# Kernel optimization log

Measured on AMD Instinct MI355X. Metric: run time of the kernel, lower is better.

Reference implementation:

```python
import jax, jax.numpy as jnp
import numpy as np
import math

D = 1024
H = 16
HD = D // H


def setup_inputs() -> dict:
    key = jax.random.key(0)
    ks = jax.random.split(key, 12)
    B, L = 2, 2048
    s = 1.0 / math.sqrt(D)
    inp = {
        "q": jax.random.normal(ks[0], (B, L, D), jnp.float32),
        "k": jax.random.normal(ks[1], (B, L, D), jnp.float32),
        "v": jax.random.normal(ks[2], (B, L, D), jnp.float32),
        "Wq": jax.random.normal(ks[3], (D, D), jnp.float32) * s,
        "bq": jnp.zeros((D,), jnp.float32),
        "Wk": jax.random.normal(ks[4], (D, D), jnp.float32) * s,
        "bk": jnp.zeros((D,), jnp.float32),
        "Wv": jax.random.normal(ks[5], (D, D), jnp.float32) * s,
        "bv": jnp.zeros((D,), jnp.float32),
        "Wo": jax.random.normal(ks[6], (D, D), jnp.float32) * s,
        "bo": jnp.zeros((D,), jnp.float32),
        "P": jax.random.normal(ks[7], (H, H), jnp.float32),  # logit_proj_pre
    }
    return inp


def _split_heads(x, B, L):
    # [B,L,D] -> [B,H,L,HD]
    return x.reshape(B, L, H, HD).transpose(0, 2, 1, 3)


def reference(q, k, v, Wq, bq, Wk, bk, Wv, bv, Wo, bo, P):
    B, L, _ = q.shape
    qh = _split_heads(q @ Wq.T + bq, B, L)
    kh = _split_heads(k @ Wk.T + bk, B, L)
    vh = _split_heads(v @ Wv.T + bv, B, L)
    # raw per-head logits [B,H,L,L]
    logits = jnp.einsum("bhld,bhmd->bhlm", qh, kh) / math.sqrt(HD)
    # talking-heads mixing across heads (pre-softmax)
    logits = jnp.einsum("bhlm,hg->bglm", logits, P)
    attn = jax.nn.softmax(logits, axis=-1)
    out = jnp.einsum("bhlm,bhmd->bhld", attn, vh)  # [B,H,L,HD]
    out = out.transpose(0, 2, 1, 3).reshape(B, L, D)
    return out @ Wo.T + bo
```

## Files before the change

### kernel.cpp

```cpp
#include <hip/hip_runtime.h>

#define D_  1024
#define H_  16
#define HD_ 64
#define L_  2048
#define B_  2
#define M_  (B_*L_)

typedef float f32x4  __attribute__((ext_vector_type(4)));
typedef short bf16x4 __attribute__((ext_vector_type(4)));
typedef short bf16x8 __attribute__((ext_vector_type(8)));

#define SRAW_PITCH 18
#define VS_PITCH   36

__device__ __forceinline__ float bf2f(short s) {
    return __uint_as_float(((unsigned int)(unsigned short)s) << 16);
}
__device__ __forceinline__ short f2bf(float f) {
    unsigned u = __float_as_uint(f);
    unsigned r = (u + 0x7FFFu + ((u >> 16) & 1u)) >> 16;
    return (short)r;
}
__device__ __forceinline__ void block_sync() {
    asm volatile("s_waitcnt lgkmcnt(0)" ::: "memory");
    __builtin_amdgcn_sched_barrier(0);
    __builtin_amdgcn_s_barrier();
    __builtin_amdgcn_sched_barrier(0);
}

__global__ __launch_bounds__(256) void proj_mfma(
    const float* __restrict__ q, const float* __restrict__ k, const float* __restrict__ v,
    const float* __restrict__ Wq, const float* __restrict__ bq,
    const float* __restrict__ Wk, const float* __restrict__ bk,
    const float* __restrict__ Wv, const float* __restrict__ bv,
    short* __restrict__ qh, short* __restrict__ qlo,
    short* __restrict__ kh, short* __restrict__ vht)
{
    const int z = blockIdx.z;
    const float* X    = (z == 0) ? q  : (z == 1) ? k  : v;
    const float* W    = (z == 0) ? Wq : (z == 1) ? Wk : Wv;
    const float* bias = (z == 0) ? bq : (z == 1) ? bk : bv;

    __shared__ short Ws[128][40];
    __shared__ short Xs[128][40];

    const int tid  = threadIdx.x;
    const int w    = tid >> 6, lane = tid & 63;
    const int l16  = lane & 15, qq = lane >> 4;
    const int m0   = blockIdx.x * 128;
    const int n0   = blockIdx.y * 128;
    const int ar0  = 64 * (w & 1);
    const int br0  = 64 * (w >> 1);

    f32x4 acc[4][4] = {};

    for (int k0 = 0; k0 < D_; k0 += 32) {
        #pragma unroll
        for (int i = 0; i < 4; ++i) {
            int fidx = i * 256 + tid;
            int r = fidx >> 3, c = fidx & 7;
            float4 wv4 = *(const float4*)(W + (size_t)(n0 + r) * D_ + k0 + c * 4);
            float4 xv4 = *(const float4*)(X + (size_t)(m0 + r) * D_ + k0 + c * 4);
            bf16x4 wb = { f2bf(wv4.x), f2bf(wv4.y), f2bf(wv4.z), f2bf(wv4.w) };
            bf16x4 xb = { f2bf(xv4.x), f2bf(xv4.y), f2bf(xv4.z), f2bf(xv4.w) };
            *(bf16x4*)&Ws[r][c * 4] = wb;
            *(bf16x4*)&Xs[r][c * 4] = xb;
        }
        __syncthreads();
        bf16x8 af[4], bfv[4];
        #pragma unroll
        for (int i = 0; i < 4; ++i) {
            const short* Ab = (z < 2) ? &Ws[ar0 + 16 * i + l16][qq * 8]
                                      : &Xs[ar0 + 16 * i + l16][qq * 8];
            const short* Bb = (z < 2) ? &Xs[br0 + 16 * i + l16][qq * 8]
                                      : &Ws[br0 + 16 * i + l16][qq * 8];
            af[i]  = *(const bf16x8*)Ab;
            bfv[i] = *(const bf16x8*)Bb;
        }
        #pragma unroll
        for (int i = 0; i < 4; ++i)
            #pragma unroll
            for (int j = 0; j < 4; ++j)
                acc[i][j] = __builtin_amdgcn_mfma_f32_16x16x32_bf16(af[i], bfv[j], acc[i][j], 0, 0, 0);
        __syncthreads();
    }

    if (z < 2) {
        #pragma unroll
        for (int i = 0; i < 4; ++i) {
            int nb = n0 + ar0 + 16 * i + qq * 4;
            float4 b4 = *(const float4*)(bias + nb);
            int h = nb >> 6, hd = nb & 63;
            #pragma unroll
            for (int j = 0; j < 4; ++j) {
                int m = m0 + br0 + 16 * j + l16;
                int bb = m >> 11, l = m & (L_ - 1);
                size_t o = ((((size_t)bb * H_ + h) * L_) + l) * HD_ + hd;
                f32x4 c = acc[i][j];
                float v0 = c[0] + b4.x, v1 = c[1] + b4.y, v2 = c[2] + b4.z, v3 = c[3] + b4.w;
                bf16x4 hi = { f2bf(v0), f2bf(v1), f2bf(v2), f2bf(v3) };
                if (z == 0) {
                    *(bf16x4*)&qh[o] = hi;
                    bf16x4 lo = { f2bf(v0 - bf2f(hi[0])), f2bf(v1 - bf2f(hi[1])),
                                  f2bf(v2 - bf2f(hi[2])), f2bf(v3 - bf2f(hi[3])) };
                    *(bf16x4*)&qlo[o] = lo;
                } else {
                    *(bf16x4*)&kh[o] = hi;
                }
            }
        }
    } else {
        #pragma unroll
        for (int i = 0; i < 4; ++i) {
            int mb = m0 + ar0 + 16 * i + qq * 4;
            int bb = mb >> 11, lb = mb & (L_ - 1);
            #pragma unroll
            for (int j = 0; j < 4; ++j) {
                int n = n0 + br0 + 16 * j + l16;
                int h = n >> 6, hd = n & 63;
                float bn = bias[n];
                size_t o = (((size_t)bb * H_ + h) * HD_ + hd) * (size_t)L_ + lb;
                f32x4 c = acc[i][j];
                bf16x4 ov = { f2bf(c[0] + bn), f2bf(c[1] + bn), f2bf(c[2] + bn), f2bf(c[3] + bn) };
                *(bf16x4*)&vht[o] = ov;
            }
        }
    }
}

__global__ __launch_bounds__(512, 2) void attn_mfma(
    const short* __restrict__ qh, const short* __restrict__ qlo,
    const short* __restrict__ kh, const short* __restrict__ vht,
    const float* __restrict__ P, short* __restrict__ attn_out)
{
    __shared__ __align__(16) float Sraw0[16 * 16 * SRAW_PITCH];
    __shared__ __align__(16) float Sraw1[16 * 16 * SRAW_PITCH];
    __shared__ __align__(16) short Vslab[8][2 * 64 * VS_PITCH];
    __shared__ float PmS[256];

    const int tid  = threadIdx.x;
    const int n    = blockIdx.x;
    const int b    = (n >> 2) & 1;
    const int l0   = ((n >> 3) * 4 + (n & 3)) * 16;
    const int w    = tid >> 6, lane = tid & 63;
    const int l16  = lane & 15, qq = lane >> 4;
    const size_t hb = (size_t)b * H_;

    bf16x8 qf[2][2][2];
    #pragma unroll
    for (int hh = 0; hh < 2; ++hh)
        #pragma unroll
        for (int kc = 0; kc < 2; ++kc) {
            size_t off = ((hb + 2 * w + hh) * L_ + l0 + l16) * HD_ + kc * 32 + qq * 8;
            qf[hh][kc][0] = *(const bf16x8*)(qh  + off);
            qf[hh][kc][1] = *(const bf16x8*)(qlo + off);
        }

    int vgi_[4], vd_[4];
    const int vc = lane & 1;
    #pragma unroll
    for (int i = 0; i < 4; ++i) {
        int vrow = i * 32 + (lane >> 1);
        vgi_[i] = vrow >> 6;
        vd_[i]  = vrow & 63;
    }
    int vwoff[4];
    #pragma unroll
    for (int i = 0; i < 4; ++i)
        vwoff[i] = vgi_[i] * (64 * VS_PITCH) + vd_[i] * VS_PITCH + vc * 8;

    bf16x8 kA[2][2], kB[2][2], vA[4], vB[4];
    #pragma unroll
    for (int hh = 0; hh < 2; ++hh)
        #pragma unroll
        for (int kc = 0; kc < 2; ++kc) {
            kA[hh][kc] = *(const bf16x8*)(kh + ((hb + 2 * w + hh) * L_ + 0  + l16) * HD_ + kc * 32 + qq * 8);
            kB[hh][kc] = *(const bf16x8*)(kh + ((hb + 2 * w + hh) * L_ + 16 + l16) * HD_ + kc * 32 + qq * 8);
        }
    #pragma unroll
    for (int i = 0; i < 4; ++i) {
        vA[i] = *(const bf16x8*)(vht + ((hb + 2 * w + vgi_[i]) * HD_ + vd_[i]) * (size_t)L_ + 0  + vc * 8);
        vB[i] = *(const bf16x8*)(vht + ((hb + 2 * w + vgi_[i]) * HD_ + vd_[i]) * (size_t)L_ + 16 + vc * 8);
    }

    if (tid < 256) PmS[tid] = P[tid] * 0.125f;

    f32x4 acc[2][4];
    #pragma unroll
    for (int dt = 0; dt < 4; ++dt) { acc[0][dt] = (f32x4){0.f,0.f,0.f,0.f}; acc[1][dt] = (f32x4){0.f,0.f,0.f,0.f}; }
    float mrun0 = 0.f, mrun1 = 0.f, srun0 = 0.f, srun1 = 0.f;

    auto qkt = [&](bf16x8 (&kr)[2][2], float* sb) {
        #pragma unroll
        for (int hh = 0; hh < 2; ++hh) {
            f32x4 s = (f32x4){0.f,0.f,0.f,0.f};
            s = __builtin_amdgcn_mfma_f32_16x16x32_bf16(kr[hh][0], qf[hh][0][0], s, 0, 0, 0);
            s = __builtin_amdgcn_mfma_f32_16x16x32_bf16(kr[hh][0], qf[hh][0][1], s, 0, 0, 0);
            s = __builtin_amdgcn_mfma_f32_16x16x32_bf16(kr[hh][1], qf[hh][1][0], s, 0, 0, 0);
            s = __builtin_amdgcn_mfma_f32_16x16x32_bf16(kr[hh][1], qf[hh][1][1], s, 0, 0, 0);
            float* sp = sb + ((2 * w + hh) * 16 + l16) * SRAW_PITCH + qq * 4;
            *(float2*)sp       = make_float2(s[0], s[1]);
            *(float2*)(sp + 2) = make_float2(s[2], s[3]);
        }
    };

    qkt(kA, Sraw0);
    block_sync();

    float pw0[16], pw1[16];
    #pragma unroll
    for (int h = 0; h < 16; ++h) {
        pw0[h] = PmS[h * 16 + 2 * w];
        pw1[h] = PmS[h * 16 + 2 * w + 1];
    }

    auto body = [&](float* sb, float* sbo, bf16x8 (&vstage)[4], bf16x8 (&kqk)[2][2],
                    bf16x8 (&kld)[2][2], bf16x8 (&vld)[4], int tnext) {
        #pragma unroll
        for (int i = 0; i < 4; ++i) {
            bf16x4 wlo = { vstage[i][0], vstage[i][1], vstage[i][2], vstage[i][3] };
            bf16x4 whi = { vstage[i][4], vstage[i][5], vstage[i][6], vstage[i][7] };
            *(bf16x4*)&Vslab[w][vwoff[i]]     = wlo;
            *(bf16x4*)&Vslab[w][vwoff[i] + 4] = whi;
        }
        {
            const int mn = tnext * 16;
            #pragma unroll
            for (int hh = 0; hh < 2; ++hh)
                #pragma unroll
                for (int kc = 0; kc < 2; ++kc)
                    kld[hh][kc] = *(const bf16x8*)(kh + ((hb + 2 * w + hh) * L_ + mn + l16) * HD_ + kc * 32 + qq * 8);
            #pragma unroll
            for (int i = 0; i < 4; ++i)
                vld[i] = *(const bf16x8*)(vht + ((hb + 2 * w + vgi_[i]) * HD_ + vd_[i]) * (size_t)L_ + mn + vc * 8);
        }
        float sx0[4] = {0.f,0.f,0.f,0.f}, sx1[4] = {0.f,0.f,0.f,0.f};
        #pragma unroll
        for (int h = 0; h < 16; ++h) {
            const float* sp = sb + (h * 16 + l16) * SRAW_PITCH + qq * 4;
            float2 ca = *(const float2*)sp;
            float2 cb = *(const float2*)(sp + 2);
            sx0[0] += pw0[h] * ca.x; sx0[1] += pw0[h] * ca.y;
            sx0[2] += pw0[h] * cb.x; sx0[3] += pw0[h] * cb.y;
            sx1[0] += pw1[h] * ca.x; sx1[1] += pw1[h] * ca.y;
            sx1[2] += pw1[h] * cb.x; sx1[3] += pw1[h] * cb.y;
        }
        float e00 = __expf(sx0[0] - mrun0), e01 = __expf(sx0[1] - mrun0);
        float e02 = __expf(sx0[2] - mrun0), e03 = __expf(sx0[3] - mrun0);
        float e10 = __expf(sx1[0] - mrun1), e11 = __expf(sx1[1] - mrun1);
        float e12 = __expf(sx1[2] - mrun1), e13 = __expf(sx1[3] - mrun1);
        bf16x4 pf0 = { f2bf(e00), f2bf(e01), f2bf(e02), f2bf(e03) };
        bf16x4 pf1 = { f2bf(e10), f2bf(e11), f2bf(e12), f2bf(e13) };
        float t0 = fmaxf(fmaxf(sx0[0], sx0[1]), fmaxf(sx0[2], sx0[3]));
        float t1 = fmaxf(fmaxf(sx1[0], sx1[1]), fmaxf(sx1[2], sx1[3]));
        t0 = fmaxf(t0, __shfl_xor(t0, 16)); t0 = fmaxf(t0, __shfl_xor(t0, 32));
        t1 = fmaxf(t1, __shfl_xor(t1, 16)); t1 = fmaxf(t1, __shfl_xor(t1, 32));
        float ps0 = e00 + e01 + e02 + e03, ps1 = e10 + e11 + e12 + e13;
        ps0 += __shfl_xor(ps0, 16); ps0 += __shfl_xor(ps0, 32);
        ps1 += __shfl_xor(ps1, 16); ps1 += __shfl_xor(ps1, 32);
        #pragma unroll
        for (int i = 0; i < 2; ++i) {
            bf16x4 pf = i ? pf1 : pf0;
            #pragma unroll
            for (int dt = 0; dt < 4; ++dt) {
                bf16x4 afr = *(const bf16x4*)&Vslab[w][i * (64 * VS_PITCH) + (dt * 16 + l16) * VS_PITCH + qq * 4];
                acc[i][dt] = __builtin_amdgcn_mfma_f32_16x16x16bf16_1k(afr, pf, acc[i][dt], 0, 0, 0);
            }
        }
        qkt(kqk, sbo);
        float mnew0 = fmaxf(mrun0, t0), mnew1 = fmaxf(mrun1, t1);
        float corr0 = __expf(mrun0 - mnew0), corr1 = __expf(mrun1 - mnew1);
        srun0 = (srun0 + ps0) * corr0; srun1 = (srun1 + ps1) * corr1;
        acc[0][0] *= corr0; acc[0][1] *= corr0; acc[0][2] *= corr0; acc[0][3] *= corr0;
        acc[1][0] *= corr1; acc[1][1] *= corr1; acc[1][2] *= corr1; acc[1][3] *= corr1;
        mrun0 = mnew0; mrun1 = mnew1;
        block_sync();
    };

    for (int itp = 0; itp < 64; ++itp) {
        const int t0 = 2 * itp;
        body(Sraw0, Sraw1, vA, kB, kA, vA, (t0 + 2) & 127);
        body(Sraw1, Sraw0, vB, kA, kB, vB, (t0 + 3) & 127);
    }

    float inv0 = 1.f / srun0, inv1 = 1.f / srun1;
    #pragma unroll
    for (int i = 0; i < 2; ++i) {
        float inv = i ? inv1 : inv0;
        #pragma unroll
        for (int dt = 0; dt < 4; ++dt) {
            f32x4 a = acc[i][dt];
            bf16x4 ov = { f2bf(a[0] * inv), f2bf(a[1] * inv), f2bf(a[2] * inv), f2bf(a[3] * inv) };
            *(bf16x4*)(attn_out + ((size_t)(b * L_ + l0 + l16)) * D_ + (2 * w + i) * 64 + dt * 16 + qq * 4) = ov;
        }
    }
}

__global__ __launch_bounds__(256) void out_mfma(
    const short* __restrict__ attn, const float* __restrict__ Wo,
    const float* __restrict__ bo, float* __restrict__ out)
{
    __shared__ short Ws[128][40];
    __shared__ short Xs[128][40];

    const int tid = threadIdx.x;
    const int w = tid >> 6, lane = tid & 63;
    const int l16 = lane & 15, qq = lane >> 4;
    const int m0 = blockIdx.x * 128;
    const int n0 = blockIdx.y * 128;
    const int ar0 = 64 * (w & 1);
    const int br0 = 64 * (w >> 1);

    f32x4 acc[4][4] = {};

    for (int k0 = 0; k0 < D_; k0 += 32) {
        #pragma unroll
        for (int i = 0; i < 4; ++i) {
            int fidx = i * 256 + tid;
            int r = fidx >> 3, c = fidx & 7;
            float4 wv4 = *(const float4*)(Wo + (size_t)(n0 + r) * D_ + k0 + c * 4);
            bf16x4 wb = { f2bf(wv4.x), f2bf(wv4.y), f2bf(wv4.z), f2bf(wv4.w) };
            *(bf16x4*)&Ws[r][c * 4] = wb;
        }
        #pragma unroll
        for (int i = 0; i < 2; ++i) {
            int cidx = i * 256 + tid;
            int r = cidx >> 2, c = cidx & 3;
            bf16x8 xv = *(const bf16x8*)(attn + (size_t)(m0 + r) * D_ + k0 + c * 8);
            *(bf16x8*)&Xs[r][c * 8] = xv;
        }
        __syncthreads();
        bf16x8 af[4], bfv[4];
        #pragma unroll
        for (int i = 0; i < 4; ++i) {
            af[i]  = *(const bf16x8*)&Ws[ar0 + 16 * i + l16][qq * 8];
            bfv[i] = *(const bf16x8*)&Xs[br0 + 16 * i + l16][qq * 8];
        }
        #pragma unroll
        for (int i = 0; i < 4; ++i)
            #pragma unroll
            for (int j = 0; j < 4; ++j)
                acc[i][j] = __builtin_amdgcn_mfma_f32_16x16x32_bf16(af[i], bfv[j], acc[i][j], 0, 0, 0);
        __syncthreads();
    }

    #pragma unroll
    for (int i = 0; i < 4; ++i) {
        int nb = n0 + ar0 + 16 * i + qq * 4;
        float4 b4 = *(const float4*)(bo + nb);
        #pragma unroll
        for (int j = 0; j < 4; ++j) {
            int m = m0 + br0 + 16 * j + l16;
            f32x4 c = acc[i][j];
            float4 ov = make_float4(c[0] + b4.x, c[1] + b4.y, c[2] + b4.z, c[3] + b4.w);
            *(float4*)&out[(size_t)m * D_ + nb] = ov;
        }
    }
}

extern "C" void kernel_launch(void* const* d_in, const int* in_sizes, int n_in,
                              void* d_out, int out_size, void* d_ws, size_t ws_size,
                              hipStream_t stream) {
    const float* q  = (const float*)d_in[0];
    const float* k  = (const float*)d_in[1];
    const float* v  = (const float*)d_in[2];
    const float* Wq = (const float*)d_in[3];
    const float* bq = (const float*)d_in[4];
    const float* Wk = (const float*)d_in[5];
    const float* bk = (const float*)d_in[6];
    const float* Wv = (const float*)d_in[7];
    const float* bv = (const float*)d_in[8];
    const float* Wo = (const float*)d_in[9];
    const float* bo = (const float*)d_in[10];
    const float* P  = (const float*)d_in[11];
    float* out = (float*)d_out;

    char* ws = (char*)d_ws;
    short* qh   = (short*)(ws);
    short* qlo  = (short*)(ws + (size_t)8 * 1024 * 1024);
    short* kh   = (short*)(ws + (size_t)16 * 1024 * 1024);
    short* vht  = (short*)(ws + (size_t)24 * 1024 * 1024);
    short* attn = (short*)(ws + (size_t)32 * 1024 * 1024);

    proj_mfma<<<dim3(M_ / 128, D_ / 128, 3), 256, 0, stream>>>(
        q, k, v, Wq, bq, Wk, bk, Wv, bv, qh, qlo, kh, vht);
    attn_mfma<<<dim3(256), 512, 0, stream>>>(qh, qlo, kh, vht, P, attn);
    out_mfma<<<dim3(M_ / 128, D_ / 128), 256, 0, stream>>>(attn, Wo, bo, out);
}
```

Before: 434.4 us.

## Compute talking-heads logit mixing with split-bf16 MFMA via shared scratch

Replaces the per-thread 16-term scalar FMA head-mixing loop with a 16x16x16 bf16 MFMA that multiplies P by the raw logits. Precision is kept through a hi/lo bf16 split using three MFMAs, and the result goes through a new Smix LDS buffer. This adds an extra block-wide barrier per tile, a transposed and likely bank-conflicting LDS read pattern, and about 18KB more shared memory. That extra LDS could reduce occupancy at 512 threads with 2 blocks per SM.

```diff
diff --git a/kernel.cpp b/kernel.cpp
--- a/kernel.cpp
+++ b/kernel.cpp
@@ -12,6 +12,7 @@
 typedef short bf16x8 __attribute__((ext_vector_type(8)));
 
 #define SRAW_PITCH 18
+#define SRAW_SLAB  (16 * SRAW_PITCH)
 #define VS_PITCH   36
 
 __device__ __forceinline__ float bf2f(short s) {
@@ -134,8 +135,9 @@
     const short* __restrict__ kh, const short* __restrict__ vht,
     const float* __restrict__ P, short* __restrict__ attn_out)
 {
-    __shared__ __align__(16) float Sraw0[16 * 16 * SRAW_PITCH];
-    __shared__ __align__(16) float Sraw1[16 * 16 * SRAW_PITCH];
+    __shared__ __align__(16) float Sraw0[16 * SRAW_SLAB];
+    __shared__ __align__(16) float Sraw1[16 * SRAW_SLAB];
+    __shared__ __align__(16) float Smix[16 * SRAW_SLAB];
     __shared__ __align__(16) short Vslab[8][2 * 64 * VS_PITCH];
     __shared__ float PmS[256];
 
@@ -208,14 +210,39 @@
     qkt(kA, Sraw0);
     block_sync();
 
-    float pw0[16], pw1[16];
-    #pragma unroll
-    for (int h = 0; h < 16; ++h) {
-        pw0[h] = PmS[h * 16 + 2 * w];
-        pw1[h] = PmS[h * 16 + 2 * w + 1];
-    }
-
-    auto body = [&](float* sb, float* sbo, bf16x8 (&vstage)[4], bf16x8 (&kqk)[2][2],
+    bf16x4 PAhi, PAlo;
+    {
+        float p0 = PmS[(qq * 4 + 0) * 16 + l16];
+        float p1 = PmS[(qq * 4 + 1) * 16 + l16];
+        float p2 = PmS[(qq * 4 + 2) * 16 + l16];
+        float p3 = PmS[(qq * 4 + 3) * 16 + l16];
+        PAhi = (bf16x4){ f2bf(p0), f2bf(p1), f2bf(p2), f2bf(p3) };
+        PAlo = (bf16x4){ f2bf(p0 - bf2f(PAhi[0])), f2bf(p1 - bf2f(PAhi[1])),
+                         f2bf(p2 - bf2f(PAhi[2])), f2bf(p3 - bf2f(PAhi[3])) };
+    }
+
+    auto mixmfma = [&](const float* sb) {
+        #pragma unroll
+        for (int mi = 0; mi < 2; ++mi) {
+            const int m = 2 * w + mi;
+            float sv0 = sb[(qq * 4 + 0) * SRAW_SLAB + l16 * SRAW_PITCH + m];
+            float sv1 = sb[(qq * 4 + 1) * SRAW_SLAB + l16 * SRAW_PITCH + m];
+            float sv2 = sb[(qq * 4 + 2) * SRAW_SLAB + l16 * SRAW_PITCH + m];
+            float sv3 = sb[(qq * 4 + 3) * SRAW_SLAB + l16 * SRAW_PITCH + m];
+            bf16x4 bhi = { f2bf(sv0), f2bf(sv1), f2bf(sv2), f2bf(sv3) };
+            bf16x4 blo = { f2bf(sv0 - bf2f(bhi[0])), f2bf(sv1 - bf2f(bhi[1])),
+                           f2bf(sv2 - bf2f(bhi[2])), f2bf(sv3 - bf2f(bhi[3])) };
+            f32x4 c = (f32x4){0.f, 0.f, 0.f, 0.f};
+            c = __builtin_amdgcn_mfma_f32_16x16x16bf16_1k(PAhi, bhi, c, 0, 0, 0);
+            c = __builtin_amdgcn_mfma_f32_16x16x16bf16_1k(PAhi, blo, c, 0, 0, 0);
+            c = __builtin_amdgcn_mfma_f32_16x16x16bf16_1k(PAlo, bhi, c, 0, 0, 0);
+            float* sp = Smix + m * SRAW_SLAB + l16 * SRAW_PITCH + qq * 4;
+            *(float2*)sp       = make_float2(c[0], c[1]);
+            *(float2*)(sp + 2) = make_float2(c[2], c[3]);
+        }
+    };
+
+    auto body = [&](const float* sb, float* sbo, bf16x8 (&vstage)[4], bf16x8 (&kqk)[2][2],
                     bf16x8 (&kld)[2][2], bf16x8 (&vld)[4], int tnext) {
         #pragma unroll
         for (int i = 0; i < 4; ++i) {
@@ -235,16 +262,14 @@
             for (int i = 0; i < 4; ++i)
                 vld[i] = *(const bf16x8*)(vht + ((hb + 2 * w + vgi_[i]) * HD_ + vd_[i]) * (size_t)L_ + mn + vc * 8);
         }
-        float sx0[4] = {0.f,0.f,0.f,0.f}, sx1[4] = {0.f,0.f,0.f,0.f};
-        #pragma unroll
-        for (int h = 0; h < 16; ++h) {
-            const float* sp = sb + (h * 16 + l16) * SRAW_PITCH + qq * 4;
-            float2 ca = *(const float2*)sp;
-            float2 cb = *(const float2*)(sp + 2);
-            sx0[0] += pw0[h] * ca.x; sx0[1] += pw0[h] * ca.y;
-            sx0[2] += pw0[h] * cb.x; sx0[3] += pw0[h] * cb.y;
-            sx1[0] += pw1[h] * ca.x; sx1[1] += pw1[h] * ca.y;
-            sx1[2] += pw1[h] * cb.x; sx1[3] += pw1[h] * cb.y;
+        mixmfma(sb);
+        block_sync();
+        float sx0[4], sx1[4];
+        #pragma unroll
+        for (int j = 0; j < 4; ++j) {
+            const float* mp = Smix + (qq * 4 + j) * SRAW_SLAB + l16 * SRAW_PITCH;
+            sx0[j] = mp[2 * w];
+            sx1[j] = mp[2 * w + 1];
         }
         float e00 = __expf(sx0[0] - mrun0), e01 = __expf(sx0[1] - mrun0);
         float e02 = __expf(sx0[2] - mrun0), e03 = __expf(sx0[3] - mrun0);
```

Result: faster. 408.1 us (-6.0%).
